# Performance work log

Measured on AMD Instinct MI355X. Metric: run time of the kernel, lower is better.

The kernel has to match this reference:

```python
import jax, jax.numpy as jnp
import numpy as np

B, P, T, V, H, E, C = 256, 256, 32, 3433, 512, 300, 128


def _gru(x, h, W_ih, W_hh, b_ih, b_hh):
    # torch.nn.GRUCell math (bias=True default)
    gx = x @ W_ih.T + b_ih          # (B, 3H)
    gh = h @ W_hh.T + b_hh          # (B, 3H)
    xr, xz, xn = jnp.split(gx, 3, axis=-1)
    hr, hz, hn = jnp.split(gh, 3, axis=-1)
    r = jax.nn.sigmoid(xr + hr)
    z = jax.nn.sigmoid(xz + hz)
    n = jnp.tanh(xn + r * hn)
    return (1.0 - z) * n + z * h


def setup_inputs() -> dict:
    key = jax.random.key(0)
    ks = jax.random.split(key, 24)
    s = 0.02
    inp = {
        'word_embs': jax.random.normal(ks[0], (B, T, E), jnp.float32),
        't_feat': jax.random.normal(ks[1], (B, C), jnp.float32),
        'c_feats': jax.random.normal(ks[2], (B, P, C), jnp.float32),
        'num_words': T,
        # top-down unit (all Linears bias=False)
        'W_td1': jax.random.normal(ks[3], (128, H), jnp.float32) * s,
        'W_td2': jax.random.normal(ks[4], (128, C), jnp.float32) * s,
        'W_td3': jax.random.normal(ks[5], (128, E), jnp.float32) * s,
        'W_td':  jax.random.normal(ks[6], (128, 128), jnp.float32) * s,
        'W1_ih': jax.random.normal(ks[7], (3 * H, 128), jnp.float32) * s,
        'W1_hh': jax.random.normal(ks[8], (3 * H, H), jnp.float32) * s,
        'b1_ih': jax.random.normal(ks[9], (3 * H,), jnp.float32) * s,
        'b1_hh': jax.random.normal(ks[10], (3 * H,), jnp.float32) * s,
        # additive attention
        'W_feat': jax.random.normal(ks[11], (H, C), jnp.float32) * s,
        'W_hidd': jax.random.normal(ks[12], (H, H), jnp.float32) * s,
        'W_att':  jax.random.normal(ks[13], (1, H), jnp.float32) * s,
        # language unit
        'W_l1': jax.random.normal(ks[14], (128, C), jnp.float32) * s,
        'W_l2': jax.random.normal(ks[15], (128, H), jnp.float32) * s,
        'W_l':  jax.random.normal(ks[16], (128, 128), jnp.float32) * s,
        'W2_ih': jax.random.normal(ks[17], (3 * H, 128), jnp.float32) * s,
        'W2_hh': jax.random.normal(ks[18], (3 * H, H), jnp.float32) * s,
        'b2_ih': jax.random.normal(ks[19], (3 * H,), jnp.float32) * s,
        'b2_hh': jax.random.normal(ks[20], (3 * H,), jnp.float32) * s,
        # classifier (bias=True)
        'W_cls': jax.random.normal(ks[21], (V, H), jnp.float32) * s,
        'b_cls': jax.random.normal(ks[22], (V,), jnp.float32) * s,
    }
    return inp


def reference(word_embs, t_feat, c_feats, num_words,
              W_td1, W_td2, W_td3, W_td, W1_ih, W1_hh, b1_ih, b1_hh,
              W_feat, W_hidd, W_att, W_l1, W_l2, W_l,
              W2_ih, W2_hh, b2_ih, b2_hh, W_cls, b_cls):
    n_steps = num_words - 1  # python int, static
    # precompute attention key projection of proposals: (B, P, H)
    feat_proj = jnp.einsum('bpc,hc->bph', c_feats, W_feat)
    td_t = t_feat @ W_td2.T  # (B, 128), time-invariant

    def step_fn(carry, x_t):
        h1, h2 = carry
        # top-down input
        s = x_t @ W_td3.T + h2 @ W_td1.T + td_t
        s = jax.nn.relu(jnp.tanh(s) @ W_td.T)
        h1 = _gru(s, h1, W1_ih, W1_hh, b1_ih, b1_hh)
        # additive attention over proposals
        comb = jnp.tanh(feat_proj + (h1 @ W_hidd.T)[:, None, :])  # (B, P, H)
        scores = jnp.einsum('bph,h->bp', comb, W_att[0])           # (B, P)
        mask = jax.nn.softmax(scores, axis=1)                      # (B, P)
        attended = jnp.einsum('bpc,bp->bc', c_feats, mask)         # (B, C)
        # language input
        l = jnp.tanh(attended @ W_l1.T + h1 @ W_l2.T)
        l = jax.nn.relu(l @ W_l.T)
        h2 = _gru(l, h2, W2_ih, W2_hh, b2_ih, b2_hh)
        logits = h2 @ W_cls.T + b_cls                              # (B, V)
        return (h1, h2), (logits, mask)

    h0 = (jnp.zeros((word_embs.shape[0], H), word_embs.dtype),
          jnp.zeros((word_embs.shape[0], H), word_embs.dtype))
    xs = jnp.swapaxes(word_embs[:, :n_steps], 0, 1)  # (T-1, B, E)
    _, (logits, masks) = jax.lax.scan(step_fn, h0, xs)
    lang_cap = jnp.swapaxes(logits, 0, 1)            # (B, T-1, V)
    topdown_attn = jnp.transpose(masks, (1, 2, 0))   # (B, P, T-1)
    return lang_cap, topdown_attn
```

## Files before the change

### kernel.cpp

```cpp
#include <hip/hip_runtime.h>
#include <hip/hip_bf16.h>

namespace {

constexpr int kB  = 256;
constexpr int kP  = 256;
constexpr int kT  = 32;
constexpr int kNS = 31;
constexpr int kV  = 3433;
constexpr int kH  = 512;
constexpr int kE  = 300;
constexpr int kC  = 128;
constexpr int kG  = 1536;

typedef __bf16 bf16x8 __attribute__((ext_vector_type(8)));
typedef float f32x4 __attribute__((ext_vector_type(4)));

__device__ __forceinline__ float fexp2(float x) {
  float r; asm("v_exp_f32 %0, %1" : "=v"(r) : "v"(x)); return r;
}
__device__ __forceinline__ float frcp(float x) {
  float r; asm("v_rcp_f32 %0, %1" : "=v"(r) : "v"(x)); return r;
}
__device__ __forceinline__ float ftanh(float x) {
  float e = fexp2(x * 2.8853900817779268f);
  return 1.0f - 2.0f * frcp(e + 1.0f);
}
__device__ __forceinline__ float fsigm(float x) {
  return frcp(1.0f + fexp2(x * -1.4426950408889634f));
}
__device__ __forceinline__ unsigned short f2bf(float f) {
  unsigned u = __float_as_uint(f);
  u += 0x7FFFu + ((u >> 16) & 1u);
  return (unsigned short)(u >> 16);
}
__device__ __forceinline__ float bf2f(unsigned short s) {
  return __uint_as_float((unsigned)s << 16);
}

__global__ void k_transpose(const float* s0, const float* s1, const float* s2,
                            const float* s3, const float* s4, const float* s5,
                            const float* s6, const float* s7, const float* s8,
                            float* d0, float* d1, float* d2, float* d3,
                            float* d4, float* d5, float* d6, float* d7,
                            float* d8) {
  const float* src; float* dst; int R, Cd;
  switch (blockIdx.y) {
    case 0:  src = s0; dst = d0; R = 128;  Cd = 300; break;
    case 1:  src = s1; dst = d1; R = 128;  Cd = 512; break;
    case 2:  src = s2; dst = d2; R = 128;  Cd = 128; break;
    case 3:  src = s3; dst = d3; R = 128;  Cd = 128; break;
    case 4:  src = s4; dst = d4; R = 128;  Cd = 512; break;
    case 5:  src = s5; dst = d5; R = 128;  Cd = 128; break;
    case 6:  src = s6; dst = d6; R = 1536; Cd = 128; break;
    case 7:  src = s7; dst = d7; R = 1536; Cd = 128; break;
    default: src = s8; dst = d8; R = 512;  Cd = 512; break;
  }
  int n = R * Cd;
  for (int i = blockIdx.x * blockDim.x + threadIdx.x; i < n;
       i += gridDim.x * blockDim.x) {
    int k = i / R, r = i - k * R;
    dst[i] = src[r * Cd + k];
  }
}

__global__ void k_tobf16(const float* s0, const float* s1, const float* s2,
                         const float* s3, const float* s4, const float* s5,
                         const float* s6, const float* s7,
                         unsigned short* d0, unsigned short* d1,
                         unsigned short* d2, unsigned short* d3,
                         unsigned short* d4, unsigned short* d5,
                         unsigned short* d6, unsigned short* d7) {
  const float* s; unsigned short* d; int n;
  switch (blockIdx.y) {
    case 0:  s = s0; d = d0; n = kC * kC; break;
    case 1:  s = s1; d = d1; n = kH * kC; break;
    case 2:  s = s2; d = d2; n = kC * kC; break;
    case 3:  s = s3; d = d3; n = kC * kG; break;
    case 4:  s = s4; d = d4; n = kH * kH; break;
    case 5:  s = s5; d = d5; n = kH * kC; break;
    case 6:  s = s6; d = d6; n = kC * kC; break;
    default: s = s7; d = d7; n = kC * kG; break;
  }
  for (int i = blockIdx.x * blockDim.x + threadIdx.x; i < n;
       i += gridDim.x * blockDim.x)
    d[i] = f2bf(s[i]);
}

__global__ void k_split(const float* s0, const float* s1, const float* s2,
                        const float* s3,
                        unsigned short* h0, unsigned short* l0,
                        unsigned short* h1, unsigned short* l1,
                        unsigned short* h2, unsigned short* l2,
                        unsigned short* h3, unsigned short* l3) {
  const float* s; unsigned short* h; unsigned short* l; int n;
  switch (blockIdx.y) {
    case 0:  s = s0; h = h0; l = l0; n = kG * kH; break;
    case 1:  s = s1; h = h1; l = l1; n = kG * kH; break;
    case 2:  s = s2; h = h2; l = l2; n = kV * kH; break;
    default: s = s3; h = h3; l = l3; n = kH * kC; break;
  }
  for (int i = blockIdx.x * blockDim.x + threadIdx.x; i < n;
       i += gridDim.x * blockDim.x) {
    float v = s[i];
    unsigned short hb = f2bf(v);
    h[i] = hb;
    l[i] = f2bf(v - bf2f(hb));
  }
}

__global__ void k_init(const float* __restrict__ t_feat,
                       const float* __restrict__ W_td2,
                       float* __restrict__ td, float* __restrict__ h1,
                       float* __restrict__ h2,
                       unsigned short* __restrict__ h1h,
                       unsigned short* __restrict__ h1l,
                       unsigned short* __restrict__ h2h,
                       unsigned short* __restrict__ h2l) {
  int tid = blockIdx.x * 256 + threadIdx.x;
  int b = tid >> 7, c = tid & 127;
  const float* tf = t_feat + b * kC;
  const float* w  = W_td2 + c * kC;
  float acc = 0.f;
  for (int k = 0; k < kC; ++k) acc = fmaf(tf[k], w[k], acc);
  td[tid] = acc;
  for (int i = tid; i < kB * kH; i += (1 << 15)) {
    h1[i] = 0.f; h2[i] = 0.f;
    h1h[i] = 0; h1l[i] = 0; h2h[i] = 0; h2l[i] = 0;
  }
}

__global__ __launch_bounds__(256) void k_xw(
    const float* __restrict__ word_embs, const float* __restrict__ td3t,
    const float* __restrict__ td, float* __restrict__ xw) {
  __shared__ float xl[4 * 300];
  __shared__ float tdl[512];
  int t = blockIdx.y, b0 = blockIdx.x * 4, tid = threadIdx.x;
  #pragma unroll
  for (int r = 0; r < 4; ++r) {
    const float* xs = word_embs + (size_t)(b0 + r) * (kT * kE) + (size_t)t * kE;
    for (int e = tid; e < kE; e += 256) xl[r * kE + e] = xs[e];
  }
  for (int i = tid; i < 512; i += 256) tdl[i] = td[(size_t)b0 * kC + i];
  __syncthreads();
  #pragma unroll
  for (int q = 0; q < 2; ++q) {
    int idx = tid + q * 256;
    int r = idx >> 7, c = idx & 127;
    float acc = tdl[idx];
    const float* xr = xl + r * kE;
    const float* w3 = td3t + c;
    for (int e = 0; e < kE; ++e) acc = fmaf(xr[e], w3[(size_t)e * 128], acc);
    xw[((size_t)t * kB + b0 + r) * kC + c] = acc;
  }
}

__global__ __launch_bounds__(256) void k_prestep(
    const float* __restrict__ xw, const unsigned short* __restrict__ tdbt,
    const unsigned short* __restrict__ iht1b, const float* __restrict__ b1_ih,
    float* __restrict__ gx1) {
  __shared__ float s1l[128];
  __shared__ float s2l[128];
  __shared__ float part[256];
  int b = blockIdx.x, tid = threadIdx.x;
  if (tid < 128) s1l[tid] = ftanh(xw[(size_t)b * kC + tid]);
  __syncthreads();
  {
    int c = tid & 127, g = tid >> 7;
    float s = 0.f;
    const unsigned short* w = tdbt + (size_t)(g * 64) * kC + c;
    for (int k = 0; k < 64; ++k)
      s = fmaf(s1l[g * 64 + k], bf2f(w[(size_t)k * kC]), s);
    part[g * 128 + c] = s;
  }
  __syncthreads();
  if (tid < 128) s2l[tid] = fmaxf(part[tid] + part[128 + tid], 0.f);
  __syncthreads();
  #pragma unroll
  for (int q = 0; q < 6; ++q) {
    int j = q * 256 + tid;
    float acc = b1_ih[j];
    const unsigned short* w = iht1b + j;
    for (int k = 0; k < kC; ++k)
      acc = fmaf(s2l[k], bf2f(w[(size_t)k * kG]), acc);
    gx1[(size_t)b * kG + j] = acc;
  }
}

__device__ __forceinline__ void mm_tile_lds(
    const unsigned short* __restrict__ Ah, const unsigned short* __restrict__ Al,
    const unsigned short* __restrict__ Bh,
    int m0, int n0, int K, int kbeg, int kend, int nMax, f32x4 acc[4][4],
    unsigned short* sAh, unsigned short* sAl, unsigned short* sBh) {
  int tid = threadIdx.x;
  int lane = tid & 63, wid = tid >> 6;
  int wm = (wid >> 1) * 64, wn = (wid & 1) * 64;
  int r16 = lane & 15, kq = lane >> 4;
  int rA = tid >> 2;
  int swSlot = (((tid & 3) ^ ((rA >> 1) & 3)) * 8);
  int cA = (tid & 3) * 8;
  int swr = (kq ^ ((r16 >> 1) & 3)) * 8;
  int brow0 = n0 + rA;       if (brow0 > nMax) brow0 = nMax;
  int brow1 = n0 + rA + 64;  if (brow1 > nMax) brow1 = nMax;
  for (int k0 = kbeg; k0 < kend; k0 += 32) {
    uint4 va0 = *(const uint4*)(Ah + (size_t)(m0 + rA) * K + k0 + cA);
    uint4 va1 = *(const uint4*)(Ah + (size_t)(m0 + rA + 64) * K + k0 + cA);
    uint4 vb0 = *(const uint4*)(Al + (size_t)(m0 + rA) * K + k0 + cA);
    uint4 vb1 = *(const uint4*)(Al + (size_t)(m0 + rA + 64) * K + k0 + cA);
    uint4 vc0 = *(const uint4*)(Bh + (size_t)brow0 * K + k0 + cA);
    uint4 vc1 = *(const uint4*)(Bh + (size_t)brow1 * K + k0 + cA);
    __syncthreads();
    *(uint4*)&sAh[rA * 32 + swSlot] = va0;
    *(uint4*)&sAh[(rA + 64) * 32 + swSlot] = va1;
    *(uint4*)&sAl[rA * 32 + swSlot] = vb0;
    *(uint4*)&sAl[(rA + 64) * 32 + swSlot] = vb1;
    *(uint4*)&sBh[rA * 32 + swSlot] = vc0;
    *(uint4*)&sBh[(rA + 64) * 32 + swSlot] = vc1;
    __syncthreads();
    bf16x8 ah[4], al[4], bh[4];
    #pragma unroll
    for (int i = 0; i < 4; ++i) {
      int ar = (wm + i * 16 + r16) * 32 + swr;
      int br = (wn + i * 16 + r16) * 32 + swr;
      ah[i] = *(const bf16x8*)&sAh[ar];
      al[i] = *(const bf16x8*)&sAl[ar];
      bh[i] = *(const bf16x8*)&sBh[br];
    }
    #pragma unroll
    for (int i = 0; i < 4; ++i)
      #pragma unroll
      for (int j = 0; j < 4; ++j) {
        acc[i][j] = __builtin_amdgcn_mfma_f32_16x16x32_bf16(ah[i], bh[j], acc[i][j], 0, 0, 0);
        acc[i][j] = __builtin_amdgcn_mfma_f32_16x16x32_bf16(al[i], bh[j], acc[i][j], 0, 0, 0);
      }
  }
}

__global__ __launch_bounds__(256) void k_featproj(
    const float* __restrict__ A, const unsigned short* __restrict__ Wh,
    unsigned short* __restrict__ out) {
  int lane = threadIdx.x & 63, wid = threadIdx.x >> 6;
  int wm = (wid >> 1) * 64, wn = (wid & 1) * 64;
  int r16 = lane & 15, kq = lane >> 4;
  int m0 = blockIdx.x * 128, n0 = blockIdx.y * 128;
  f32x4 acc[4][4];
  #pragma unroll
  for (int i = 0; i < 4; ++i)
    #pragma unroll
    for (int j = 0; j < 4; ++j) acc[i][j] = (f32x4){0.f, 0.f, 0.f, 0.f};
  for (int k0 = 0; k0 < kC; k0 += 32) {
    int kk = k0 + kq * 8;
    bf16x8 ah[4], al[4], bh[4];
    #pragma unroll
    for (int i = 0; i < 4; ++i) {
      const float* pa = A + (size_t)(m0 + wm + i * 16 + r16) * kC + kk;
      float4 v0 = *(const float4*)pa;
      float4 v1 = *(const float4*)(pa + 4);
      float vv[8] = {v0.x, v0.y, v0.z, v0.w, v1.x, v1.y, v1.z, v1.w};
      union { unsigned short s[8]; bf16x8 v; } uh, ul;
      #pragma unroll
      for (int q = 0; q < 8; ++q) {
        unsigned short hb = f2bf(vv[q]);
        uh.s[q] = hb;
        ul.s[q] = f2bf(vv[q] - bf2f(hb));
      }
      ah[i] = uh.v; al[i] = ul.v;
      const unsigned short* pb = Wh + (size_t)(n0 + wn + i * 16 + r16) * kC + kk;
      union { uint4 u; bf16x8 v; } xb;
      xb.u = *(const uint4*)pb;
      bh[i] = xb.v;
    }
    #pragma unroll
    for (int i = 0; i < 4; ++i)
      #pragma unroll
      for (int j = 0; j < 4; ++j) {
        acc[i][j] = __builtin_amdgcn_mfma_f32_16x16x32_bf16(ah[i], bh[j], acc[i][j], 0, 0, 0);
        acc[i][j] = __builtin_amdgcn_mfma_f32_16x16x32_bf16(al[i], bh[j], acc[i][j], 0, 0, 0);
      }
  }
  #pragma unroll
  for (int i = 0; i < 4; ++i)
    #pragma unroll
    for (int j = 0; j < 4; ++j)
      #pragma unroll
      for (int r = 0; r < 4; ++r) {
        int m = m0 + wm + i * 16 + kq * 4 + r;
        int n = n0 + wn + j * 16 + r16;
        out[(size_t)m * kH + n] = f2bf(acc[i][j][r]);
      }
}

__global__ __launch_bounds__(256) void k_gh(
    const unsigned short* __restrict__ h1h, const unsigned short* __restrict__ h1l,
    const unsigned short* __restrict__ h2h, const unsigned short* __restrict__ h2l,
    const unsigned short* __restrict__ w1hh_h, const unsigned short* __restrict__ w2hh_h,
    const float* __restrict__ b1_hh, const float* __restrict__ b2_hh,
    float* __restrict__ gh1, float* __restrict__ gh2) {
  __shared__ __align__(16) unsigned short sAh[4096], sAl[4096], sBh[4096];
  int g2 = blockIdx.x;
  int half = g2 & 1, g = g2 >> 1;
  const unsigned short *Ah, *Al, *Wh; const float* bias; float* out;
  if (g < 24) { Ah = h1h; Al = h1l; Wh = w1hh_h; bias = b1_hh; out = gh1; }
  else { g -= 24; Ah = h2h; Al = h2l; Wh = w2hh_h; bias = b2_hh; out = gh2; }
  out += (size_t)half * (kB * kG);
  int m0 = (g / 12) * 128, n0 = (g % 12) * 128;
  f32x4 acc[4][4];
  #pragma unroll
  for (int i = 0; i < 4; ++i)
    #pragma unroll
    for (int j = 0; j < 4; ++j) acc[i][j] = (f32x4){0.f, 0.f, 0.f, 0.f};
  mm_tile_lds(Ah, Al, Wh, m0, n0, kH, half * 256, half * 256 + 256,
              kG - 1, acc, sAh, sAl, sBh);
  int tid = threadIdx.x;
  int lane = tid & 63, wid = tid >> 6;
  int wm = (wid >> 1) * 64, wn = (wid & 1) * 64;
  int r16 = lane & 15, kq = lane >> 4;
  #pragma unroll
  for (int i = 0; i < 4; ++i)
    #pragma unroll
    for (int j = 0; j < 4; ++j)
      #pragma unroll
      for (int r = 0; r < 4; ++r) {
        int m = m0 + wm + i * 16 + kq * 4 + r;
        int n = n0 + wn + j * 16 + r16;
        float v = acc[i][j][r];
        if (half == 0) v += bias[n];
        out[(size_t)m * kG + n] = v;
      }
}

__global__ __launch_bounds__(1024, 4) void k_step2(
    float* __restrict__ gx1, const float* __restrict__ gh1,
    const float* __restrict__ gh2,
    float* __restrict__ h1, float* __restrict__ h2,
    unsigned short* __restrict__ h1h, unsigned short* __restrict__ h1l,
    unsigned short* __restrict__ h2h, unsigned short* __restrict__ h2l,
    const unsigned short* __restrict__ whdbT, const float* __restrict__ W_att,
    const unsigned short* __restrict__ fp, const float* __restrict__ c_feats,
    const unsigned short* __restrict__ l1bt, const unsigned short* __restrict__ l2bt,
    const unsigned short* __restrict__ lbt, const unsigned short* __restrict__ iht2b,
    const float* __restrict__ b2_ih,
    const unsigned short* __restrict__ td1bt, const unsigned short* __restrict__ tdbt,
    const unsigned short* __restrict__ iht1b, const float* __restrict__ b1_ih,
    const float* __restrict__ xw,
    unsigned short* __restrict__ h2all_h, unsigned short* __restrict__ h2all_l,
    float* __restrict__ mask_ws, int t) {
  __shared__ float partbuf[8192];
  __shared__ float h1p[512];
  __shared__ float h2p[512];
  __shared__ float hqs[512];
  __shared__ float scs[256];
  __shared__ float red[16];
  __shared__ float red2[16];
  __shared__ float attl[128];
  __shared__ float lt1[128];
  __shared__ float llv[128];
  __shared__ float s1l[128];
  __shared__ float s2l[128];
  __shared__ float gx2l[1536];
  const int b = blockIdx.x;
  const int tid = threadIdx.x;
  const int lane = tid & 63, wv = tid >> 6;
  const size_t GPART = (size_t)kB * kG;

  if (tid < 512) {
    int c = tid;
    float gr = gx1[(size_t)b * kG + c];
    float gz = gx1[(size_t)b * kG + 512 + c];
    float gn = gx1[(size_t)b * kG + 1024 + c];
    float hr = gh1[(size_t)b * kG + c] + gh1[GPART + (size_t)b * kG + c];
    float hz = gh1[(size_t)b * kG + 512 + c] + gh1[GPART + (size_t)b * kG + 512 + c];
    float hnv = gh1[(size_t)b * kG + 1024 + c] + gh1[GPART + (size_t)b * kG + 1024 + c];
    float rr = fsigm(gr + hr);
    float zz = fsigm(gz + hz);
    float nn = ftanh(gn + rr * hnv);
    float ho = h1[(size_t)b * kH + c];
    float hn = (1.f - zz) * nn + zz * ho;
    h1[(size_t)b * kH + c] = hn;
    h1p[c] = hn;
    unsigned short hb = f2bf(hn);
    h1h[(size_t)b * kH + c] = hb;
    h1l[(size_t)b * kH + c] = f2bf(hn - bf2f(hb));
  }
  __syncthreads();

  {
    int cg = tid & 63, kg = tid >> 6;
    int c0 = cg * 8;
    const unsigned short* w = whdbT + (size_t)(kg * 32) * kH + c0;
    float acc[8] = {};
    #pragma unroll 4
    for (int k = 0; k < 32; ++k) {
      union { uint4 u; unsigned short s[8]; } wu;
      wu.u = *(const uint4*)(w + (size_t)k * kH);
      float h = h1p[kg * 32 + k];
      #pragma unroll
      for (int j = 0; j < 8; ++j) acc[j] = fmaf(h, bf2f(wu.s[j]), acc[j]);
    }
    float* pp = &partbuf[kg * 512 + c0];
    #pragma unroll
    for (int j = 0; j < 8; ++j) pp[j] = acc[j];
  }
  __syncthreads();
  if (tid < 512) {
    float s = 0.f;
    #pragma unroll
    for (int g = 0; g < 16; ++g) s += partbuf[g * 512 + tid];
    hqs[tid] = s;
  }
  __syncthreads();

  {
    float hq8[8], aw[8];
    #pragma unroll
    for (int j = 0; j < 8; ++j) hq8[j] = hqs[lane * 8 + j];
    {
      float4 a0 = *(const float4*)(W_att + lane * 8);
      float4 a1 = *(const float4*)(W_att + lane * 8 + 4);
      aw[0] = a0.x; aw[1] = a0.y; aw[2] = a0.z; aw[3] = a0.w;
      aw[4] = a1.x; aw[5] = a1.y; aw[6] = a1.z; aw[7] = a1.w;
    }
    const unsigned short* fpb = fp + (size_t)b * kP * kH;
    int p0 = wv * 16;
    uint4 rv = *(const uint4*)(fpb + (size_t)p0 * kH + lane * 8);
    for (int p = p0; p < p0 + 16; ++p) {
      union { uint4 v; unsigned short s[8]; } u; u.v = rv;
      if (p + 1 < p0 + 16)
        rv = *(const uint4*)(fpb + (size_t)(p + 1) * kH + lane * 8);
      float sc = 0.f;
      #pragma unroll
      for (int j = 0; j < 8; ++j) {
        float f = __uint_as_float((unsigned)u.s[j] << 16);
        sc += aw[j] * ftanh(f + hq8[j]);
      }
      #pragma unroll
      for (int m = 32; m; m >>= 1) sc += __shfl_xor(sc, m, 64);
      if (lane == 0) scs[p] = sc;
    }
  }
  __syncthreads();

  {
    float sv = (tid < 256) ? scs[tid] : -1e30f;
    float mx = sv;
    #pragma unroll
    for (int m = 32; m; m >>= 1) mx = fmaxf(mx, __shfl_xor(mx, m, 64));
    if (lane == 0) red[wv] = mx;
    __syncthreads();
    float bm = red[0];
    #pragma unroll
    for (int i = 1; i < 16; ++i) bm = fmaxf(bm, red[i]);
    float ev = (tid < 256) ? fexp2((sv - bm) * 1.4426950408889634f) : 0.f;
    float sm = ev;
    #pragma unroll
    for (int m = 32; m; m >>= 1) sm += __shfl_xor(sm, m, 64);
    if (lane == 0) red2[wv] = sm;
    __syncthreads();
    float tot = 0.f;
    #pragma unroll
    for (int i = 0; i < 16; ++i) tot += red2[i];
    if (tid < 256) {
      float mk = ev * frcp(tot);
      scs[tid] = mk;
      mask_ws[(size_t)t * (kB * kP) + (size_t)b * kP + tid] = mk;
    }
  }
  __syncthreads();

  {
    int c = tid & 127, q = tid >> 7;
    const float* cf = c_feats + ((size_t)b * kP + q * 32) * kC + c;
    const float* ms = scs + q * 32;
    float acc = 0.f;
    for (int p = 0; p < 32; ++p) acc = fmaf(ms[p], cf[(size_t)p * kC], acc);
    partbuf[q * 128 + c] = acc;
  }
  __syncthreads();
  if (tid < 128) {
    float s = 0.f;
    #pragma unroll
    for (int q = 0; q < 8; ++q) s += partbuf[q * 128 + tid];
    attl[tid] = s;
  }
  __syncthreads();

  {
    if (tid < 512) {
      int cg = tid & 15, kg = tid >> 4;
      int c0 = cg * 8;
      const unsigned short* w = l2bt + (size_t)(kg * 16) * kC + c0;
      float acc[8] = {};
      for (int k = 0; k < 16; ++k) {
        union { uint4 u; unsigned short s[8]; } wu;
        wu.u = *(const uint4*)(w + (size_t)k * kC);
        float h = h1p[kg * 16 + k];
        #pragma unroll
        for (int j = 0; j < 8; ++j) acc[j] = fmaf(h, bf2f(wu.s[j]), acc[j]);
      }
      float* pp = &partbuf[kg * 128 + c0];
      #pragma unroll
      for (int j = 0; j < 8; ++j) pp[j] = acc[j];
    } else if (tid < 768) {
      int tt = tid - 512;
      int cg = tt & 15, kg = tt >> 4;
      int c0 = cg * 8;
      const unsigned short* w = l1bt + (size_t)(kg * 8) * kC + c0;
      float acc[8] = {};
      for (int k = 0; k < 8; ++k) {
        union { uint4 u; unsigned short s[8]; } wu;
        wu.u = *(const uint4*)(w + (size_t)k * kC);
        float a = attl[kg * 8 + k];
        #pragma unroll
        for (int j = 0; j < 8; ++j) acc[j] = fmaf(a, bf2f(wu.s[j]), acc[j]);
      }
      float* pp = &partbuf[4096 + kg * 128 + c0];
      #pragma unroll
      for (int j = 0; j < 8; ++j) pp[j] = acc[j];
    }
  }
  __syncthreads();
  if (tid < 128) {
    float s = 0.f;
    #pragma unroll
    for (int g = 0; g < 32; ++g) s += partbuf[g * 128 + tid];
    #pragma unroll
    for (int g = 0; g < 16; ++g) s += partbuf[4096 + g * 128 + tid];
    lt1[tid] = ftanh(s);
  }
  __syncthreads();

  if (tid < 256) {
    int cg = tid & 15, kg = tid >> 4;
    int c0 = cg * 8;
    const unsigned short* w = lbt + (size_t)(kg * 8) * kC + c0;
    float acc[8] = {};
    for (int k = 0; k < 8; ++k) {
      union { uint4 u; unsigned short s[8]; } wu;
      wu.u = *(const uint4*)(w + (size_t)k * kC);
      float l = lt1[kg * 8 + k];
      #pragma unroll
      for (int j = 0; j < 8; ++j) acc[j] = fmaf(l, bf2f(wu.s[j]), acc[j]);
    }
    float* pp = &partbuf[kg * 128 + c0];
    #pragma unroll
    for (int j = 0; j < 8; ++j) pp[j] = acc[j];
  }
  __syncthreads();
  if (tid < 128) {
    float s = 0.f;
    #pragma unroll
    for (int g = 0; g < 16; ++g) s += partbuf[g * 128 + tid];
    llv[tid] = fmaxf(s, 0.f);
  }
  __syncthreads();

  if (tid < 768) {
    int cg = tid % 192, kg = tid / 192;
    int c0 = cg * 8;
    const unsigned short* w = iht2b + (size_t)(kg * 32) * kG + c0;
    float acc[8] = {};
    #pragma unroll 4
    for (int k = 0; k < 32; ++k) {
      union { uint4 u; unsigned short s[8]; } wu;
      wu.u = *(const uint4*)(w + (size_t)k * kG);
      float l = llv[kg * 32 + k];
      #pragma unroll
      for (int j = 0; j < 8; ++j) acc[j] = fmaf(l, bf2f(wu.s[j]), acc[j]);
    }
    float* pp = &partbuf[kg * 1536 + c0];
    #pragma unroll
    for (int j = 0; j < 8; ++j) pp[j] = acc[j];
  }
  __syncthreads();
  for (int c = tid; c < kG; c += 1024) {
    float s = b2_ih[c];
    #pragma unroll
    for (int g = 0; g < 4; ++g) s += partbuf[g * 1536 + c];
    gx2l[c] = s;
  }
  __syncthreads();
  if (tid < 512) {
    int c = tid;
    float ghr = gh2[(size_t)b * kG + c] + gh2[GPART + (size_t)b * kG + c];
    float ghz = gh2[(size_t)b * kG + 512 + c] + gh2[GPART + (size_t)b * kG + 512 + c];
    float ghn = gh2[(size_t)b * kG + 1024 + c] + gh2[GPART + (size_t)b * kG + 1024 + c];
    float rr = fsigm(gx2l[c] + ghr);
    float zz = fsigm(gx2l[512 + c] + ghz);
    float nn = ftanh(gx2l[1024 + c] + rr * ghn);
    float ho = h2[(size_t)b * kH + c];
    float hn = (1.f - zz) * nn + zz * ho;
    h2[(size_t)b * kH + c] = hn;
    h2p[c] = hn;
    unsigned short hb = f2bf(hn);
    unsigned short lb = f2bf(hn - bf2f(hb));
    h2h[(size_t)b * kH + c] = hb;
    h2l[(size_t)b * kH + c] = lb;
    size_t o = ((size_t)t * kB + b) * kH + c;
    h2all_h[o] = hb;
    h2all_l[o] = lb;
  }
  __syncthreads();

  if (t + 1 < kNS) {
    if (tid < 512) {
      int cg = tid & 15, kg = tid >> 4;
      int c0 = cg * 8;
      const unsigned short* w = td1bt + (size_t)(kg * 16) * kC + c0;
      float acc[8] = {};
      for (int k = 0; k < 16; ++k) {
        union { uint4 u; unsigned short s[8]; } wu;
        wu.u = *(const uint4*)(w + (size_t)k * kC);
        float h = h2p[kg * 16 + k];
        #pragma unroll
        for (int j = 0; j < 8; ++j) acc[j] = fmaf(h, bf2f(wu.s[j]), acc[j]);
      }
      float* pp = &partbuf[kg * 128 + c0];
      #pragma unroll
      for (int j = 0; j < 8; ++j) pp[j] = acc[j];
    }
    __syncthreads();
    if (tid < 128) {
      float s = xw[((size_t)(t + 1) * kB + b) * kC + tid];
      #pragma unroll
      for (int g = 0; g < 32; ++g) s += partbuf[g * 128 + tid];
      s1l[tid] = ftanh(s);
    }
    __syncthreads();
    if (tid < 256) {
      int cg = tid & 15, kg = tid >> 4;
      int c0 = cg * 8;
      const unsigned short* w = tdbt + (size_t)(kg * 8) * kC + c0;
      float acc[8] = {};
      for (int k = 0; k < 8; ++k) {
        union { uint4 u; unsigned short s[8]; } wu;
        wu.u = *(const uint4*)(w + (size_t)k * kC);
        float sv = s1l[kg * 8 + k];
        #pragma unroll
        for (int j = 0; j < 8; ++j) acc[j] = fmaf(sv, bf2f(wu.s[j]), acc[j]);
      }
      float* pp = &partbuf[kg * 128 + c0];
      #pragma unroll
      for (int j = 0; j < 8; ++j) pp[j] = acc[j];
    }
    __syncthreads();
    if (tid < 128) {
      float s = 0.f;
      #pragma unroll
      for (int g = 0; g < 16; ++g) s += partbuf[g * 128 + tid];
      s2l[tid] = fmaxf(s, 0.f);
    }
    __syncthreads();
    if (tid < 768) {
      int cg = tid % 192, kg = tid / 192;
      int c0 = cg * 8;
      const unsigned short* w = iht1b + (size_t)(kg * 32) * kG + c0;
      float acc[8] = {};
      #pragma unroll 4
      for (int k = 0; k < 32; ++k) {
        union { uint4 u; unsigned short s[8]; } wu;
        wu.u = *(const uint4*)(w + (size_t)k * kG);
        float sv = s2l[kg * 32 + k];
        #pragma unroll
        for (int j = 0; j < 8; ++j) acc[j] = fmaf(sv, bf2f(wu.s[j]), acc[j]);
      }
      float* pp = &partbuf[kg * 1536 + c0];
      #pragma unroll
      for (int j = 0; j < 8; ++j) pp[j] = acc[j];
    }
    __syncthreads();
    for (int c = tid; c < kG; c += 1024) {
      float s = b1_ih[c];
      #pragma unroll
      for (int g = 0; g < 4; ++g) s += partbuf[g * 1536 + c];
      gx1[(size_t)b * kG + c] = s;
    }
  }
}

__global__ __launch_bounds__(256) void k_atrans(
    const float* __restrict__ mws, float* __restrict__ attn_out) {
  __shared__ float tile[256][33];
  int pair0 = blockIdx.x * 256;
  int tid = threadIdx.x;
  #pragma unroll
  for (int t = 0; t < kNS; ++t)
    tile[tid][t] = mws[(size_t)t * (kB * kP) + pair0 + tid];
  __syncthreads();
  float* outb = attn_out + (size_t)pair0 * kNS;
  #pragma unroll
  for (int i = 0; i < kNS; ++i) {
    int g = i * 256 + tid;
    int pr = g / 31, tt = g - pr * 31;
    outb[g] = tile[pr][tt];
  }
}

__global__ __launch_bounds__(256) void k_cls(
    const unsigned short* __restrict__ Ah, const unsigned short* __restrict__ Al,
    const unsigned short* __restrict__ Wh,
    const float* __restrict__ bc, float* __restrict__ out) {
  __shared__ __align__(16) unsigned short sAh[4096], sAl[4096], sBh[4096];
  int m0 = blockIdx.x * 128, n0 = blockIdx.y * 128;
  f32x4 acc[4][4];
  #pragma unroll
  for (int i = 0; i < 4; ++i)
    #pragma unroll
    for (int j = 0; j < 4; ++j) acc[i][j] = (f32x4){0.f, 0.f, 0.f, 0.f};
  mm_tile_lds(Ah, Al, Wh, m0, n0, kH, 0, kH, kV - 1, acc, sAh, sAl, sBh);
  int lane = threadIdx.x & 63, wid = threadIdx.x >> 6;
  int wm = (wid >> 1) * 64, wn = (wid & 1) * 64;
  int r16 = lane & 15, kq = lane >> 4;
  #pragma unroll
  for (int i = 0; i < 4; ++i)
    #pragma unroll
    for (int j = 0; j < 4; ++j)
      #pragma unroll
      for (int r = 0; r < 4; ++r) {
        int m = m0 + wm + i * 16 + kq * 4 + r;
        int n = n0 + wn + j * 16 + r16;
        if (n < kV) {
          int tt = m >> 8, b = m & 255;
          out[(size_t)b * (kNS * kV) + (size_t)tt * kV + n] = acc[i][j][r] + bc[n];
        }
      }
}

}

extern "C" void kernel_launch(void* const* d_in, const int* in_sizes, int n_in,
                              void* d_out, int out_size, void* d_ws,
                              size_t ws_size, hipStream_t stream) {
  (void)in_sizes; (void)n_in; (void)out_size; (void)ws_size;
  const float* word_embs = (const float*)d_in[0];
  const float* t_feat    = (const float*)d_in[1];
  const float* c_feats   = (const float*)d_in[2];
  const float* W_td1 = (const float*)d_in[4];
  const float* W_td2 = (const float*)d_in[5];
  const float* W_td3 = (const float*)d_in[6];
  const float* W_td  = (const float*)d_in[7];
  const float* W1_ih = (const float*)d_in[8];
  const float* W1_hh = (const float*)d_in[9];
  const float* b1_ih = (const float*)d_in[10];
  const float* b1_hh = (const float*)d_in[11];
  const float* W_feat = (const float*)d_in[12];
  const float* W_hidd = (const float*)d_in[13];
  const float* W_att  = (const float*)d_in[14];
  const float* W_l1 = (const float*)d_in[15];
  const float* W_l2 = (const float*)d_in[16];
  const float* W_l  = (const float*)d_in[17];
  const float* W2_ih = (const float*)d_in[18];
  const float* W2_hh = (const float*)d_in[19];
  const float* b2_ih = (const float*)d_in[20];
  const float* b2_hh = (const float*)d_in[21];
  const float* W_cls = (const float*)d_in[22];
  const float* b_cls = (const float*)d_in[23];

  float* lang = (float*)d_out;
  float* attn_out = lang + (size_t)kB * kNS * kV;
  unsigned short* fp = (unsigned short*)d_out;

  float* p = (float*)d_ws;
  float* h1 = p;      p += kB * kH;
  float* h2 = p;      p += kB * kH;
  float* td = p;      p += kB * kC;
  float* gx1 = p;     p += (size_t)kB * kG;
  float* gh1 = p;     p += (size_t)2 * kB * kG;
  float* gh2 = p;     p += (size_t)2 * kB * kG;
  float* mask_ws = p; p += (size_t)kNS * kB * kP;
  float* xw = p;      p += (size_t)kNS * kB * kC;
  float* td3t = p;    p += kE * 128;
  float* td1t = p;    p += kH * 128;
  float* tdt  = p;    p += 128 * 128;
  float* l1t  = p;    p += 128 * 128;
  float* l2t  = p;    p += kH * 128;
  float* lt   = p;    p += 128 * 128;
  float* iht1 = p;    p += 128 * kG;
  float* iht2 = p;    p += 128 * kG;
  float* whd_t = p;   p += kH * kH;

  unsigned short* u = (unsigned short*)p;
  unsigned short* h1h = u;     u += kB * kH;
  unsigned short* h1l = u;     u += kB * kH;
  unsigned short* h2h = u;     u += kB * kH;
  unsigned short* h2l = u;     u += kB * kH;
  unsigned short* w1hh_h = u;  u += (size_t)kG * kH;
  unsigned short* w1hh_l = u;  u += (size_t)kG * kH;
  unsigned short* w2hh_h = u;  u += (size_t)kG * kH;
  unsigned short* w2hh_l = u;  u += (size_t)kG * kH;
  unsigned short* wc_h = u;    u += (size_t)kV * kH;
  unsigned short* wc_l = u;    u += (size_t)kV * kH;
  unsigned short* wf_h = u;    u += (size_t)kH * kC;
  unsigned short* wf_l = u;    u += (size_t)kH * kC;
  unsigned short* h2all_h = u; u += (size_t)kNS * kB * kH;
  unsigned short* h2all_l = u; u += (size_t)kNS * kB * kH;
  unsigned short* l1bt = u;    u += kC * kC;
  unsigned short* l2bt = u;    u += (size_t)kH * kC;
  unsigned short* lbt = u;     u += kC * kC;
  unsigned short* iht2b = u;   u += (size_t)kC * kG;
  unsigned short* whdbT = u;   u += (size_t)kH * kH;
  unsigned short* td1bt = u;   u += (size_t)kH * kC;
  unsigned short* tdbt = u;    u += kC * kC;
  unsigned short* iht1b = u;   u += (size_t)kC * kG;

  k_transpose<<<dim3(64, 9), 256, 0, stream>>>(
      W_td3, W_td1, W_td, W_l1, W_l2, W_l, W1_ih, W2_ih, W_hidd,
      td3t, td1t, tdt, l1t, l2t, lt, iht1, iht2, whd_t);
  k_tobf16<<<dim3(96, 8), 256, 0, stream>>>(
      l1t, l2t, lt, iht2, whd_t, td1t, tdt, iht1,
      l1bt, l2bt, lbt, iht2b, whdbT, td1bt, tdbt, iht1b);
  k_split<<<dim3(256, 4), 256, 0, stream>>>(
      W1_hh, W2_hh, W_cls, W_feat,
      w1hh_h, w1hh_l, w2hh_h, w2hh_l, wc_h, wc_l, wf_h, wf_l);
  k_init<<<128, 256, 0, stream>>>(t_feat, W_td2, td, h1, h2,
                                  h1h, h1l, h2h, h2l);
  k_featproj<<<dim3(512, 4), 256, 0, stream>>>(c_feats, wf_h, fp);
  k_xw<<<dim3(64, kNS), 256, 0, stream>>>(word_embs, td3t, td, xw);
  k_prestep<<<256, 256, 0, stream>>>(xw, tdbt, iht1b, b1_ih, gx1);

  for (int t = 0; t < kNS; ++t) {
    k_gh<<<96, 256, 0, stream>>>(h1h, h1l, h2h, h2l,
                                 w1hh_h, w2hh_h, b1_hh, b2_hh, gh1, gh2);
    k_step2<<<256, 1024, 0, stream>>>(gx1, gh1, gh2, h1, h2,
                                      h1h, h1l, h2h, h2l, whdbT, W_att, fp,
                                      c_feats, l1bt, l2bt, lbt, iht2b, b2_ih,
                                      td1bt, tdbt, iht1b, b1_ih, xw,
                                      h2all_h, h2all_l, mask_ws, t);
  }
  k_atrans<<<256, 256, 0, stream>>>(mask_ws, attn_out);
  k_cls<<<dim3(62, 27), 256, 0, stream>>>(h2all_h, h2all_l, wc_h,
                                          b_cls, lang);
}
```

Baseline: 2.115 ms.

## Move GRU1 input projection into MFMA gh kernel and prefetch tile loads

The per-sample scalar W1_ih projection inside k_step2 and k_prestep is replaced by writing the bf16 hi/lo split of the s2 activation. The gx1 = s2·W1_ihᵀ + b1_ih product is now computed as extra MFMA tiles inside k_gh, which grows from 96 to 120 blocks. The shared tile loader also register-prefetches the next K slice before the MFMA loop, overlapping global loads with compute. This trades per-block LDS reductions in the large step kernel for a batched matrix multiply, at the cost of an extra global round trip for s2. The unused iht1 transpose output is now pointed at scratch space at the start of the workspace.

```diff
diff --git a/kernel.cpp b/kernel.cpp
--- a/kernel.cpp
+++ b/kernel.cpp
@@ -80,7 +80,7 @@
     case 4:  s = s4; d = d4; n = kH * kH; break;
     case 5:  s = s5; d = d5; n = kH * kC; break;
     case 6:  s = s6; d = d6; n = kC * kC; break;
-    default: s = s7; d = d7; n = kC * kG; break;
+    default: s = s7; d = d7; n = kG * kC; break;
   }
   for (int i = blockIdx.x * blockDim.x + threadIdx.x; i < n;
        i += gridDim.x * blockDim.x)
@@ -157,10 +157,8 @@
 
 __global__ __launch_bounds__(256) void k_prestep(
     const float* __restrict__ xw, const unsigned short* __restrict__ tdbt,
-    const unsigned short* __restrict__ iht1b, const float* __restrict__ b1_ih,
-    float* __restrict__ gx1) {
+    unsigned short* __restrict__ s2h, unsigned short* __restrict__ s2l) {
   __shared__ float s1l[128];
-  __shared__ float s2l[128];
   __shared__ float part[256];
   int b = blockIdx.x, tid = threadIdx.x;
   if (tid < 128) s1l[tid] = ftanh(xw[(size_t)b * kC + tid]);
@@ -174,16 +172,11 @@
     part[g * 128 + c] = s;
   }
   __syncthreads();
-  if (tid < 128) s2l[tid] = fmaxf(part[tid] + part[128 + tid], 0.f);
-  __syncthreads();
-  #pragma unroll
-  for (int q = 0; q < 6; ++q) {
-    int j = q * 256 + tid;
-    float acc = b1_ih[j];
-    const unsigned short* w = iht1b + j;
-    for (int k = 0; k < kC; ++k)
-      acc = fmaf(s2l[k], bf2f(w[(size_t)k * kG]), acc);
-    gx1[(size_t)b * kG + j] = acc;
+  if (tid < 128) {
+    float s = fmaxf(part[tid] + part[128 + tid], 0.f);
+    unsigned short hb = f2bf(s);
+    s2h[(size_t)b * kC + tid] = hb;
+    s2l[(size_t)b * kC + tid] = f2bf(s - bf2f(hb));
   }
 }
 
@@ -202,13 +195,19 @@
   int swr = (kq ^ ((r16 >> 1) & 3)) * 8;
   int brow0 = n0 + rA;       if (brow0 > nMax) brow0 = nMax;
   int brow1 = n0 + rA + 64;  if (brow1 > nMax) brow1 = nMax;
+  const unsigned short* pa0 = Ah + (size_t)(m0 + rA) * K + cA;
+  const unsigned short* pa1 = Ah + (size_t)(m0 + rA + 64) * K + cA;
+  const unsigned short* pb0 = Al + (size_t)(m0 + rA) * K + cA;
+  const unsigned short* pb1 = Al + (size_t)(m0 + rA + 64) * K + cA;
+  const unsigned short* pc0 = Bh + (size_t)brow0 * K + cA;
+  const unsigned short* pc1 = Bh + (size_t)brow1 * K + cA;
+  uint4 va0 = *(const uint4*)(pa0 + kbeg);
+  uint4 va1 = *(const uint4*)(pa1 + kbeg);
+  uint4 vb0 = *(const uint4*)(pb0 + kbeg);
+  uint4 vb1 = *(const uint4*)(pb1 + kbeg);
+  uint4 vc0 = *(const uint4*)(pc0 + kbeg);
+  uint4 vc1 = *(const uint4*)(pc1 + kbeg);
   for (int k0 = kbeg; k0 < kend; k0 += 32) {
-    uint4 va0 = *(const uint4*)(Ah + (size_t)(m0 + rA) * K + k0 + cA);
-    uint4 va1 = *(const uint4*)(Ah + (size_t)(m0 + rA + 64) * K + k0 + cA);
-    uint4 vb0 = *(const uint4*)(Al + (size_t)(m0 + rA) * K + k0 + cA);
-    uint4 vb1 = *(const uint4*)(Al + (size_t)(m0 + rA + 64) * K + k0 + cA);
-    uint4 vc0 = *(const uint4*)(Bh + (size_t)brow0 * K + k0 + cA);
-    uint4 vc1 = *(const uint4*)(Bh + (size_t)brow1 * K + k0 + cA);
     __syncthreads();
     *(uint4*)&sAh[rA * 32 + swSlot] = va0;
     *(uint4*)&sAh[(rA + 64) * 32 + swSlot] = va1;
@@ -217,6 +216,15 @@
     *(uint4*)&sBh[rA * 32 + swSlot] = vc0;
     *(uint4*)&sBh[(rA + 64) * 32 + swSlot] = vc1;
     __syncthreads();
+    if (k0 + 32 < kend) {
+      int kn = k0 + 32;
+      va0 = *(const uint4*)(pa0 + kn);
+      va1 = *(const uint4*)(pa1 + kn);
+      vb0 = *(const uint4*)(pb0 + kn);
+      vb1 = *(const uint4*)(pb1 + kn);
+      vc0 = *(const uint4*)(pc0 + kn);
+      vc1 = *(const uint4*)(pc1 + kn);
+    }
     bf16x8 ah[4], al[4], bh[4];
     #pragma unroll
     for (int i = 0; i < 4; ++i) {
@@ -295,42 +303,61 @@
     const unsigned short* __restrict__ h2h, const unsigned short* __restrict__ h2l,
     const unsigned short* __restrict__ w1hh_h, const unsigned short* __restrict__ w2hh_h,
     const float* __restrict__ b1_hh, const float* __restrict__ b2_hh,
-    float* __restrict__ gh1, float* __restrict__ gh2) {
+    float* __restrict__ gh1, float* __restrict__ gh2,
+    const unsigned short* __restrict__ s2h, const unsigned short* __restrict__ s2l,
+    const unsigned short* __restrict__ w1ih_h, const float* __restrict__ b1_ih,
+    float* __restrict__ gx1) {
   __shared__ __align__(16) unsigned short sAh[4096], sAl[4096], sBh[4096];
-  int g2 = blockIdx.x;
-  int half = g2 & 1, g = g2 >> 1;
-  const unsigned short *Ah, *Al, *Wh; const float* bias; float* out;
-  if (g < 24) { Ah = h1h; Al = h1l; Wh = w1hh_h; bias = b1_hh; out = gh1; }
-  else { g -= 24; Ah = h2h; Al = h2l; Wh = w2hh_h; bias = b2_hh; out = gh2; }
-  out += (size_t)half * (kB * kG);
-  int m0 = (g / 12) * 128, n0 = (g % 12) * 128;
+  int blk = blockIdx.x, tid = threadIdx.x;
+  int lane = tid & 63, wid = tid >> 6;
+  int wm = (wid >> 1) * 64, wn = (wid & 1) * 64;
+  int r16 = lane & 15, kq = lane >> 4;
   f32x4 acc[4][4];
   #pragma unroll
   for (int i = 0; i < 4; ++i)
     #pragma unroll
     for (int j = 0; j < 4; ++j) acc[i][j] = (f32x4){0.f, 0.f, 0.f, 0.f};
-  mm_tile_lds(Ah, Al, Wh, m0, n0, kH, half * 256, half * 256 + 256,
-              kG - 1, acc, sAh, sAl, sBh);
-  int tid = threadIdx.x;
-  int lane = tid & 63, wid = tid >> 6;
-  int wm = (wid >> 1) * 64, wn = (wid & 1) * 64;
-  int r16 = lane & 15, kq = lane >> 4;
-  #pragma unroll
-  for (int i = 0; i < 4; ++i)
-    #pragma unroll
-    for (int j = 0; j < 4; ++j)
-      #pragma unroll
-      for (int r = 0; r < 4; ++r) {
-        int m = m0 + wm + i * 16 + kq * 4 + r;
-        int n = n0 + wn + j * 16 + r16;
-        float v = acc[i][j][r];
-        if (half == 0) v += bias[n];
-        out[(size_t)m * kG + n] = v;
-      }
+  if (blk < 96) {
+    int half = blk & 1, g = blk >> 1;
+    const unsigned short *Ah, *Al, *Wh; const float* bias; float* out;
+    if (g < 24) { Ah = h1h; Al = h1l; Wh = w1hh_h; bias = b1_hh; out = gh1; }
+    else { g -= 24; Ah = h2h; Al = h2l; Wh = w2hh_h; bias = b2_hh; out = gh2; }
+    out += (size_t)half * (kB * kG);
+    int m0 = (g / 12) * 128, n0 = (g % 12) * 128;
+    mm_tile_lds(Ah, Al, Wh, m0, n0, kH, half * 256, half * 256 + 256,
+                kG - 1, acc, sAh, sAl, sBh);
+    #pragma unroll
+    for (int i = 0; i < 4; ++i)
+      #pragma unroll
+      for (int j = 0; j < 4; ++j)
+        #pragma unroll
+        for (int r = 0; r < 4; ++r) {
+          int m = m0 + wm + i * 16 + kq * 4 + r;
+          int n = n0 + wn + j * 16 + r16;
+          float v = acc[i][j][r];
+          if (half == 0) v += bias[n];
+          out[(size_t)m * kG + n] = v;
+        }
+  } else {
+    int gg = blk - 96;
+    int m0 = (gg / 12) * 128, n0 = (gg % 12) * 128;
+    mm_tile_lds(s2h, s2l, w1ih_h, m0, n0, kC, 0, kC, kG - 1, acc,
+                sAh, sAl, sBh);
+    #pragma unroll
+    for (int i = 0; i < 4; ++i)
+      #pragma unroll
+      for (int j = 0; j < 4; ++j)
+        #pragma unroll
+        for (int r = 0; r < 4; ++r) {
+          int m = m0 + wm + i * 16 + kq * 4 + r;
+          int n = n0 + wn + j * 16 + r16;
+          gx1[(size_t)m * kG + n] = acc[i][j][r] + b1_ih[n];
+        }
+  }
 }
 
 __global__ __launch_bounds__(1024, 4) void k_step2(
-    float* __restrict__ gx1, const float* __restrict__ gh1,
+    const float* __restrict__ gx1, const float* __restrict__ gh1,
     const float* __restrict__ gh2,
     float* __restrict__ h1, float* __restrict__ h2,
     unsigned short* __restrict__ h1h, unsigned short* __restrict__ h1l,
@@ -341,8 +368,8 @@
     const unsigned short* __restrict__ lbt, const unsigned short* __restrict__ iht2b,
     const float* __restrict__ b2_ih,
     const unsigned short* __restrict__ td1bt, const unsigned short* __restrict__ tdbt,
-    const unsigned short* __restrict__ iht1b, const float* __restrict__ b1_ih,
     const float* __restrict__ xw,
+    unsigned short* __restrict__ s2h, unsigned short* __restrict__ s2l,
     unsigned short* __restrict__ h2all_h, unsigned short* __restrict__ h2all_l,
     float* __restrict__ mask_ws, int t) {
   __shared__ float partbuf[8192];
@@ -356,7 +383,6 @@
   __shared__ float lt1[128];
   __shared__ float llv[128];
   __shared__ float s1l[128];
-  __shared__ float s2l[128];
   __shared__ float gx2l[1536];
   const int b = blockIdx.x;
   const int tid = threadIdx.x;
@@ -647,32 +673,10 @@
       float s = 0.f;
       #pragma unroll
       for (int g = 0; g < 16; ++g) s += partbuf[g * 128 + tid];
-      s2l[tid] = fmaxf(s, 0.f);
-    }
-    __syncthreads();
-    if (tid < 768) {
-      int cg = tid % 192, kg = tid / 192;
-      int c0 = cg * 8;
-      const unsigned short* w = iht1b + (size_t)(kg * 32) * kG + c0;
-      float acc[8] = {};
-      #pragma unroll 4
-      for (int k = 0; k < 32; ++k) {
-        union { uint4 u; unsigned short s[8]; } wu;
-        wu.u = *(const uint4*)(w + (size_t)k * kG);
-        float sv = s2l[kg * 32 + k];
-        #pragma unroll
-        for (int j = 0; j < 8; ++j) acc[j] = fmaf(sv, bf2f(wu.s[j]), acc[j]);
-      }
-      float* pp = &partbuf[kg * 1536 + c0];
-      #pragma unroll
-      for (int j = 0; j < 8; ++j) pp[j] = acc[j];
-    }
-    __syncthreads();
-    for (int c = tid; c < kG; c += 1024) {
-      float s = b1_ih[c];
-      #pragma unroll
-      for (int g = 0; g < 4; ++g) s += partbuf[g * 1536 + c];
-      gx1[(size_t)b * kG + c] = s;
+      s = fmaxf(s, 0.f);
+      unsigned short hb = f2bf(s);
+      s2h[(size_t)b * kC + tid] = hb;
+      s2l[(size_t)b * kC + tid] = f2bf(s - bf2f(hb));
     }
   }
 }
@@ -774,7 +778,6 @@
   float* l1t  = p;    p += 128 * 128;
   float* l2t  = p;    p += kH * 128;
   float* lt   = p;    p += 128 * 128;
-  float* iht1 = p;    p += 128 * kG;
   float* iht2 = p;    p += 128 * kG;
   float* whd_t = p;   p += kH * kH;
 
@@ -800,14 +803,16 @@
   unsigned short* whdbT = u;   u += (size_t)kH * kH;
   unsigned short* td1bt = u;   u += (size_t)kH * kC;
   unsigned short* tdbt = u;    u += kC * kC;
-  unsigned short* iht1b = u;   u += (size_t)kC * kG;
+  unsigned short* w1ih_h = u;  u += (size_t)kG * kC;
+  unsigned short* s2h = u;     u += kB * kC;
+  unsigned short* s2l = u;     u += kB * kC;
 
   k_transpose<<<dim3(64, 9), 256, 0, stream>>>(
       W_td3, W_td1, W_td, W_l1, W_l2, W_l, W1_ih, W2_ih, W_hidd,
-      td3t, td1t, tdt, l1t, l2t, lt, iht1, iht2, whd_t);
+      td3t, td1t, tdt, l1t, l2t, lt, (float*)d_ws , iht2, whd_t);
   k_tobf16<<<dim3(96, 8), 256, 0, stream>>>(
-      l1t, l2t, lt, iht2, whd_t, td1t, tdt, iht1,
-      l1bt, l2bt, lbt, iht2b, whdbT, td1bt, tdbt, iht1b);
+      l1t, l2t, lt, iht2, whd_t, td1t, tdt, W1_ih,
+      l1bt, l2bt, lbt, iht2b, whdbT, td1bt, tdbt, w1ih_h);
   k_split<<<dim3(256, 4), 256, 0, stream>>>(
       W1_hh, W2_hh, W_cls, W_feat,
       w1hh_h, w1hh_l, w2hh_h, w2hh_l, wc_h, wc_l, wf_h, wf_l);
@@ -815,15 +820,16 @@
                                   h1h, h1l, h2h, h2l);
   k_featproj<<<dim3(512, 4), 256, 0, stream>>>(c_feats, wf_h, fp);
   k_xw<<<dim3(64, kNS), 256, 0, stream>>>(word_embs, td3t, td, xw);
-  k_prestep<<<256, 256, 0, stream>>>(xw, tdbt, iht1b, b1_ih, gx1);
+  k_prestep<<<256, 256, 0, stream>>>(xw, tdbt, s2h, s2l);
 
   for (int t = 0; t < kNS; ++t) {
-    k_gh<<<96, 256, 0, stream>>>(h1h, h1l, h2h, h2l,
-                                 w1hh_h, w2hh_h, b1_hh, b2_hh, gh1, gh2);
+    k_gh<<<120, 256, 0, stream>>>(h1h, h1l, h2h, h2l,
+                                  w1hh_h, w2hh_h, b1_hh, b2_hh, gh1, gh2,
+                                  s2h, s2l, w1ih_h, b1_ih, gx1);
     k_step2<<<256, 1024, 0, stream>>>(gx1, gh1, gh2, h1, h2,
                                       h1h, h1l, h2h, h2l, whdbT, W_att, fp,
                                       c_feats, l1bt, l2bt, lbt, iht2b, b2_ih,
-                                      td1bt, tdbt, iht1b, b1_ih, xw,
+                                      td1bt, tdbt, xw, s2h, s2l,
                                       h2all_h, h2all_l, mask_ws, t);
   }
   k_atrans<<<256, 256, 0, stream>>>(mask_ws, attn_out);
```

Result: faster. 1.915 ms (-9.4%).
